# Optimization experiments

Hardware: AMD Instinct MI355X
Metric: run time of the kernel (lower is better)

The kernel has to match this reference:

```python
import jax, jax.numpy as jnp
import numpy as np

B, S, E, H, T, K, F = 2, 2048, 768, 12, 128, 16, 3072
DH = E // H


def _ln(x, s, b, eps=1e-6):
    mu = jnp.mean(x, axis=-1, keepdims=True)
    var = jnp.mean(jnp.square(x - mu), axis=-1, keepdims=True)
    return (x - mu) * jax.lax.rsqrt(var + eps) * s + b


def _forward(h, mask, W_topo, b_topo, W_m1, b_m1, W_m2, b_m2, ln_t_s, ln_t_b,
             W_p1, b_p1, W_p2, b_p2, ln1_s, ln1_b, Wq, Wk, Wv, W_gate, b_gate,
             W_o, b_o, ln2_s, ln2_b, W_f1, b_f1, W_f2, b_f2):
    # ---- TopologicalFeatureExtractor (on pre-LN hidden_states) ----
    topo = h @ W_topo + b_topo                                   # [B,S,T]
    hn = h / (jnp.linalg.norm(h, axis=-1, keepdims=True) + 1e-8)
    dist = 1.0 - jnp.einsum('bsd,btd->bst', hn, hn)              # cosine distance [B,S,S]
    dist = jnp.where(jnp.eye(S, dtype=bool)[None], 1e9, dist)    # mask self
    idx = jnp.argsort(dist, axis=-1)[:, :, :K]                   # k-NN indices [B,S,K]
    nd = jnp.take_along_axis(dist, idx, axis=-1)                 # [B,S,K]
    nf = jax.vmap(lambda t, i: t[i])(topo, idx)                  # gather neighbors [B,S,K,T]
    wts = jax.nn.softmax(-nd, axis=-1)[..., None]
    combined = topo + (nf * wts).sum(axis=2)
    t = jax.nn.relu(combined @ W_m1 + b_m1) @ W_m2 + b_m2
    t = _ln(t, ln_t_s, ln_t_b)
    pf = jax.nn.relu(t @ W_p1 + b_p1) @ W_p2 + b_p2              # persistence features [B,S,T]
    # ---- TopologicalAttention (pre-LN residual block) ----
    x = _ln(h, ln1_s, ln1_b)
    q = (x @ Wq).reshape(B, S, H, DH)
    k = (x @ Wk).reshape(B, S, H, DH)
    v = (x @ Wv).reshape(B, S, H, DH)
    scores = jnp.einsum('bqhd,bkhd->bhqk', q, k) / jnp.sqrt(jnp.asarray(DH, jnp.float32))
    scores = jnp.where(mask[:, None, None, :] == 0, -10000.0, scores)
    probs = jax.nn.softmax(scores, axis=-1)
    ctx = jnp.einsum('bhqk,bkhd->bqhd', probs, v).reshape(B, S, E)
    gate = jax.nn.sigmoid(jnp.concatenate([ctx, pf], axis=-1) @ W_gate + b_gate)
    ctx = gate * ctx + (1.0 - gate) * x                          # x is attention's input (post-LN)
    h = h + (ctx @ W_o + b_o)
    # ---- FFN block ----
    y = _ln(h, ln2_s, ln2_b)
    y = jax.nn.gelu(y @ W_f1 + b_f1, approximate=True)
    return h + (y @ W_f2 + b_f2)


def setup_inputs() -> dict:
    key = jax.random.key(0)
    ks = jax.random.split(key, 16)
    w = lambda k, shp: (0.02 * jax.random.normal(k, shp)).astype(jnp.float32)
    z = lambda shp: jnp.zeros(shp, jnp.float32)
    o = lambda shp: jnp.ones(shp, jnp.float32)
    return {
        'hidden_states': jax.random.normal(ks[0], (B, S, E), jnp.float32),
        'attention_mask': jnp.ones((B, S), jnp.int32),
        'W_topo': w(ks[1], (E, T)), 'b_topo': z((T,)),
        'W_m1': w(ks[2], (T, 2 * T)), 'b_m1': z((2 * T,)),
        'W_m2': w(ks[3], (2 * T, T)), 'b_m2': z((T,)),
        'ln_t_s': o((T,)), 'ln_t_b': z((T,)),
        'W_p1': w(ks[4], (T, T)), 'b_p1': z((T,)),
        'W_p2': w(ks[5], (T, T)), 'b_p2': z((T,)),
        'ln1_s': o((E,)), 'ln1_b': z((E,)),
        'Wq': w(ks[6], (E, E)), 'Wk': w(ks[7], (E, E)), 'Wv': w(ks[8], (E, E)),
        'W_gate': w(ks[9], (E + T, E)), 'b_gate': z((E,)),
        'W_o': w(ks[10], (E, E)), 'b_o': z((E,)),
        'ln2_s': o((E,)), 'ln2_b': z((E,)),
        'W_f1': w(ks[11], (E, F)), 'b_f1': z((F,)),
        'W_f2': w(ks[12], (F, E)), 'b_f2': z((E,)),
    }


def reference(hidden_states, attention_mask, W_topo, b_topo, W_m1, b_m1, W_m2, b_m2,
              ln_t_s, ln_t_b, W_p1, b_p1, W_p2, b_p2, ln1_s, ln1_b, Wq, Wk, Wv,
              W_gate, b_gate, W_o, b_o, ln2_s, ln2_b, W_f1, b_f1, W_f2, b_f2):
    return _forward(hidden_states, attention_mask, W_topo, b_topo, W_m1, b_m1, W_m2, b_m2,
                    ln_t_s, ln_t_b, W_p1, b_p1, W_p2, b_p2, ln1_s, ln1_b, Wq, Wk, Wv,
                    W_gate, b_gate, W_o, b_o, ln2_s, ln2_b, W_f1, b_f1, W_f2, b_f2)
```

## Files before the change

kernel.cpp:

```cpp
#include <hip/hip_runtime.h>
#include <hip/hip_bf16.h>
#include <math.h>

#define BDIM 2
#define SDIM 2048
#define EDIM 768
#define HDIM 12
#define TDIM 128
#define KNN  16
#define FDIM 3072
#define DHD  64
#define BS   (BDIM*SDIM)

typedef __attribute__((ext_vector_type(8))) short short8;
typedef __attribute__((ext_vector_type(4))) float f32x4;

__device__ __forceinline__ short f2bf(float f) {
  unsigned u = __float_as_uint(f);
  u = u + 0x7fff + ((u >> 16) & 1);
  return (short)(u >> 16);
}
__device__ __forceinline__ float bf2f(short s) {
  return __uint_as_float(((unsigned)(unsigned short)s) << 16);
}
__device__ __forceinline__ void cp16(void* lds, const void* g) {
  __builtin_amdgcn_global_load_lds(
      (const __attribute__((address_space(1))) unsigned int*)g,
      (__attribute__((address_space(3))) unsigned int*)lds, 16, 0, 0);
}

__device__ __forceinline__ void block_reduce_sum2(float& a, float& b) {
  __shared__ float sa[4], sb[4];
  #pragma unroll
  for (int off = 32; off > 0; off >>= 1) {
    a += __shfl_xor(a, off);
    b += __shfl_xor(b, off);
  }
  int wid = threadIdx.x >> 6;
  if ((threadIdx.x & 63) == 0) { sa[wid] = a; sb[wid] = b; }
  __syncthreads();
  a = sa[0] + sa[1] + sa[2] + sa[3];
  b = sb[0] + sb[1] + sb[2] + sb[3];
}

__global__ __launch_bounds__(256) void cvt_bf_kernel(
    const float* __restrict__ in, short* __restrict__ outp, int n8) {
  int i = blockIdx.x*256 + threadIdx.x;
  if (i < n8) {
    const float4* p4 = (const float4*)(in + (size_t)i*8);
    float4 a = p4[0], b = p4[1];
    short8 pk;
    pk[0]=f2bf(a.x); pk[1]=f2bf(a.y); pk[2]=f2bf(a.z); pk[3]=f2bf(a.w);
    pk[4]=f2bf(b.x); pk[5]=f2bf(b.y); pk[6]=f2bf(b.z); pk[7]=f2bf(b.w);
    *(short8*)(outp + (size_t)i*8) = pk;
  }
}

__global__ __launch_bounds__(256) void wconv_kernel(
    const float* __restrict__ W, short* __restrict__ Wt, int K, int N) {
  __shared__ float tile[64][65];
  const int n0 = blockIdx.x*64, k0 = blockIdx.y*64;
  const int tid = threadIdx.x;
  for (int i = tid; i < 4096; i += 256) {
    int r = i>>6, c = i&63;
    tile[r][c] = W[(size_t)(k0+r)*N + n0 + c];
  }
  __syncthreads();
  for (int i = tid; i < 4096; i += 256) {
    int r = i>>6, c = i&63;
    Wt[(size_t)(n0+r)*K + k0 + c] = f2bf(tile[c][r]);
  }
}

__global__ __launch_bounds__(256) void vtrans_kernel(
    const short* __restrict__ qkv, short* __restrict__ vt) {
  __shared__ short t[64][72];
  const int s0 = blockIdx.x*64;
  const int bh = blockIdx.y;
  const int b = bh / HDIM, h = bh % HDIM;
  const int tid = threadIdx.x;
  for (int i = tid; i < 512; i += 256) {
    int r = i>>3, c8 = (i&7)<<3;
    *(short8*)&t[r][c8] =
        *(const short8*)&qkv[(size_t)(b*SDIM+s0+r)*2304 + 1536 + h*DHD + c8];
  }
  __syncthreads();
  for (int i = tid; i < 512; i += 256) {
    int d = i>>3, c8 = (i&7)<<3;
    short8 pk;
    #pragma unroll
    for (int j = 0; j < 8; ++j) pk[j] = t[c8+j][d];
    *(short8*)&vt[(size_t)(bh*DHD+d)*SDIM + s0 + c8] = pk;
  }
}

__global__ __launch_bounds__(256) void norm_ln1_kernel(
    const float* __restrict__ h, const float* __restrict__ s,
    const float* __restrict__ bb, short* __restrict__ hh, short* __restrict__ hl,
    float* __restrict__ x, short* __restrict__ xb) {
  int row = blockIdx.x;
  const float* hr = h + (size_t)row * EDIM;
  float v[3], s1 = 0.f, s2 = 0.f;
  #pragma unroll
  for (int t = 0; t < 3; ++t) {
    v[t] = hr[threadIdx.x + 256*t];
    s1 += v[t]; s2 += v[t]*v[t];
  }
  block_reduce_sum2(s1, s2);
  float mu  = s1 * (1.f/EDIM);
  float var = s2 * (1.f/EDIM) - mu*mu;
  float rs  = rsqrtf(var + 1e-6f);
  float invn = 1.f / (sqrtf(s2) + 1e-8f);
  #pragma unroll
  for (int t = 0; t < 3; ++t) {
    int i = threadIdx.x + 256*t;
    size_t idx = (size_t)row*EDIM + i;
    float hnv = v[t]*invn;
    short hi = f2bf(hnv);
    hh[idx] = hi;
    hl[idx] = f2bf(hnv - bf2f(hi));
    float xv = (v[t]-mu)*rs*s[i] + bb[i];
    x[idx] = xv;
    xb[idx] = f2bf(xv);
  }
}

__global__ __launch_bounds__(256) void ln_bf_kernel(
    const float* __restrict__ in, const float* __restrict__ s,
    const float* __restrict__ bb, short* __restrict__ outb) {
  int row = blockIdx.x;
  const float* r = in + (size_t)row * EDIM;
  float v[3], s1 = 0.f, s2 = 0.f;
  #pragma unroll
  for (int t = 0; t < 3; ++t) {
    v[t] = r[threadIdx.x + 256*t];
    s1 += v[t]; s2 += v[t]*v[t];
  }
  block_reduce_sum2(s1, s2);
  float mu  = s1 * (1.f/EDIM);
  float var = s2 * (1.f/EDIM) - mu*mu;
  float rs  = rsqrtf(var + 1e-6f);
  #pragma unroll
  for (int t = 0; t < 3; ++t) {
    int i = threadIdx.x + 256*t;
    outb[(size_t)row*EDIM + i] = f2bf((v[t]-mu)*rs*s[i] + bb[i]);
  }
}

template<int ACT, int OUTBF>
__global__ __launch_bounds__(256) void gemm_mfma(
    const short* __restrict__ A, const short* __restrict__ Wt,
    const float* __restrict__ bias, const float* res,
    float* Cf, short* Cb, int Cb_ld,
    const float* __restrict__ blc, const float* __restrict__ blx,
    int K, int N) {
  __shared__ __align__(16) short As[128*64];
  __shared__ __align__(16) short Bs[128*64];
  const int bm = blockIdx.y*128, bn = blockIdx.x*128;
  const int tid = threadIdx.x;
  const int w = tid>>6, lane = tid&63, l15 = lane&15, g = lane>>4;
  const int wm = (w>>1)*64, wn = (w&1)*64;
  f32x4 acc[4][4] = {};
  for (int k0 = 0; k0 < K; k0 += 64) {
    #pragma unroll
    for (int it = 0; it < 4; ++it) {
      int p = (it*256 + tid)*16;
      int row = p >> 7;
      int slot = (p >> 4) & 7;
      int ss = slot ^ (row & 7);
      cp16((char*)As + it*4096 + w*1024, A  + (size_t)(bm+row)*K + k0 + ss*8);
      cp16((char*)Bs + it*4096 + w*1024, Wt + (size_t)(bn+row)*K + k0 + ss*8);
    }
    __syncthreads();
    #pragma unroll
    for (int ks = 0; ks < 2; ++ks) {
      short8 af[4], bfv[4];
      #pragma unroll
      for (int mt = 0; mt < 4; ++mt) {
        int r = wm + mt*16 + l15;
        af[mt] = *(const short8*)&As[r*64 + (((ks*4+g) ^ (r&7))*8)];
      }
      #pragma unroll
      for (int nt = 0; nt < 4; ++nt) {
        int r = wn + nt*16 + l15;
        bfv[nt] = *(const short8*)&Bs[r*64 + (((ks*4+g) ^ (r&7))*8)];
      }
      #pragma unroll
      for (int mt = 0; mt < 4; ++mt)
        #pragma unroll
        for (int nt = 0; nt < 4; ++nt)
          acc[mt][nt] = __builtin_amdgcn_mfma_f32_16x16x32_bf16(af[mt], bfv[nt], acc[mt][nt], 0, 0, 0);
    }
    __syncthreads();
  }
  #pragma unroll
  for (int mt = 0; mt < 4; ++mt) {
    #pragma unroll
    for (int nt = 0; nt < 4; ++nt) {
      #pragma unroll
      for (int reg = 0; reg < 4; ++reg) {
        int row = bm + wm + mt*16 + g*4 + reg;
        int col = bn + wn + nt*16 + l15;
        float v = acc[mt][nt][reg];
        if (bias) v += bias[col];
        if (ACT == 2) {
          float xx = v;
          float t2 = 0.7978845608028654f*(xx + 0.044715f*xx*xx*xx);
          v = 0.5f*xx*(1.f + tanhf(t2));
        }
        if (ACT == 3) {
          float gg = 1.f/(1.f + expf(-v));
          size_t ix = (size_t)row*EDIM + col;
          float mv = gg*blc[ix] + (1.f-gg)*blx[ix];
          Cb[(size_t)row*Cb_ld + col] = f2bf(mv);
        } else {
          if (res) v += res[(size_t)row*N + col];
          if (OUTBF) Cb[(size_t)row*Cb_ld + col] = f2bf(v);
          else       Cf[(size_t)row*N + col] = v;
        }
      }
    }
  }
}

__global__ __launch_bounds__(256) void dist_mfma(
    const short* __restrict__ Hh, const short* __restrict__ Hl,
    float* __restrict__ dist) {
  __shared__ __align__(16) short Ah[128*64], Al[128*64];
  __shared__ __align__(16) short Bh[128*64], Bl[128*64];
  const int bm = blockIdx.y*128, bn = blockIdx.x*128;
  const int tid = threadIdx.x;
  const int w = tid>>6, lane = tid&63, l15 = lane&15, g = lane>>4;
  const int wm = (w>>1)*64, wn = (w&1)*64;
  f32x4 acc[4][4] = {};
  for (int k0 = 0; k0 < EDIM; k0 += 64) {
    #pragma unroll
    for (int it = 0; it < 4; ++it) {
      int p = (it*256 + tid)*16;
      int row = p >> 7;
      int slot = (p >> 4) & 7;
      int ss = slot ^ (row & 7);
      size_t ga = (size_t)(bm+row)*EDIM + k0 + ss*8;
      size_t gb = (size_t)(bn+row)*EDIM + k0 + ss*8;
      cp16((char*)Ah + it*4096 + w*1024, Hh + ga);
      cp16((char*)Al + it*4096 + w*1024, Hl + ga);
      cp16((char*)Bh + it*4096 + w*1024, Hh + gb);
      cp16((char*)Bl + it*4096 + w*1024, Hl + gb);
    }
    __syncthreads();
    #pragma unroll
    for (int ks = 0; ks < 2; ++ks) {
      short8 ah[4], al[4], bh[4], bl[4];
      #pragma unroll
      for (int mt = 0; mt < 4; ++mt) {
        int r = wm + mt*16 + l15;
        int o = r*64 + (((ks*4+g) ^ (r&7))*8);
        ah[mt] = *(const short8*)&Ah[o];
        al[mt] = *(const short8*)&Al[o];
      }
      #pragma unroll
      for (int nt = 0; nt < 4; ++nt) {
        int r = wn + nt*16 + l15;
        int o = r*64 + (((ks*4+g) ^ (r&7))*8);
        bh[nt] = *(const short8*)&Bh[o];
        bl[nt] = *(const short8*)&Bl[o];
      }
      #pragma unroll
      for (int mt = 0; mt < 4; ++mt)
        #pragma unroll
        for (int nt = 0; nt < 4; ++nt) {
          acc[mt][nt] = __builtin_amdgcn_mfma_f32_16x16x32_bf16(ah[mt], bh[nt], acc[mt][nt], 0, 0, 0);
          acc[mt][nt] = __builtin_amdgcn_mfma_f32_16x16x32_bf16(ah[mt], bl[nt], acc[mt][nt], 0, 0, 0);
          acc[mt][nt] = __builtin_amdgcn_mfma_f32_16x16x32_bf16(al[mt], bh[nt], acc[mt][nt], 0, 0, 0);
        }
    }
    __syncthreads();
  }
  #pragma unroll
  for (int mt = 0; mt < 4; ++mt) {
    #pragma unroll
    for (int nt = 0; nt < 4; ++nt) {
      #pragma unroll
      for (int reg = 0; reg < 4; ++reg) {
        int row = bm + wm + mt*16 + g*4 + reg;
        int col = bn + wn + nt*16 + l15;
        float v = 1.f - acc[mt][nt][reg];
        if (row == col) v = 1e9f;
        dist[(size_t)row*SDIM + col] = v;
      }
    }
  }
}

__global__ __launch_bounds__(256) void topk_kernel(
    const float* __restrict__ dist, const float* __restrict__ topob,
    float* __restrict__ combb) {
  int s = blockIdx.x;
  __shared__ float wbv[4];
  __shared__ int   wbi[4];
  __shared__ float nd[KNN];
  __shared__ int   nidx[KNN];
  __shared__ float wts[KNN];
  const int tid = threadIdx.x, lane = tid & 63, wid = tid >> 6;
  const float* drow = dist + (size_t)s*SDIM;
  float lv[8];
  float best = 3e38f; int bidx = 1<<30;
  #pragma unroll
  for (int j = 0; j < 8; ++j) {
    int i = tid + j*256;
    float v = drow[i];
    lv[j] = v;
    if (v < best) { best = v; bidx = i; }
  }
  for (int pass = 0; pass < KNN; ++pass) {
    float bv = best; int bi = bidx;
    #pragma unroll
    for (int off = 32; off > 0; off >>= 1) {
      float ov = __shfl_xor(bv, off);
      int   oi = __shfl_xor(bi, off);
      if (ov < bv || (ov == bv && oi < bi)) { bv = ov; bi = oi; }
    }
    if (lane == 0) { wbv[wid] = bv; wbi[wid] = bi; }
    __syncthreads();
    if (tid == 0) {
      float fv = wbv[0]; int fi = wbi[0];
      #pragma unroll
      for (int q2 = 1; q2 < 4; ++q2)
        if (wbv[q2] < fv || (wbv[q2] == fv && wbi[q2] < fi)) { fv = wbv[q2]; fi = wbi[q2]; }
      nd[pass] = fv; nidx[pass] = fi;
    }
    __syncthreads();
    int wi = nidx[pass];
    if ((wi & 255) == tid) {
      int jj = wi >> 8;
      #pragma unroll
      for (int j = 0; j < 8; ++j) if (j == jj) lv[j] = 3e38f;
      best = 3e38f; bidx = 1<<30;
      #pragma unroll
      for (int j = 0; j < 8; ++j)
        if (lv[j] < best) { best = lv[j]; bidx = tid + j*256; }
    }
    __syncthreads();
  }
  if (tid == 0) {
    float m = -nd[0];
    for (int k2 = 1; k2 < KNN; ++k2) m = fmaxf(m, -nd[k2]);
    float ssum = 0.f;
    for (int k2 = 0; k2 < KNN; ++k2) { float e = expf(-nd[k2] - m); wts[k2] = e; ssum += e; }
    float inv = 1.f/ssum;
    for (int k2 = 0; k2 < KNN; ++k2) wts[k2] *= inv;
  }
  __syncthreads();
  if (tid < TDIM) {
    float acc = topob[(size_t)s*TDIM + tid];
    #pragma unroll
    for (int k2 = 0; k2 < KNN; ++k2) acc += wts[k2]*topob[(size_t)nidx[k2]*TDIM + tid];
    combb[(size_t)s*TDIM + tid] = acc;
  }
}

__global__ __launch_bounds__(256) void topo_mlp_kernel(
    const float* __restrict__ comb,
    const float* __restrict__ W1, const float* __restrict__ b1,
    const float* __restrict__ W2, const float* __restrict__ b2,
    const float* __restrict__ lns, const float* __restrict__ lnb,
    const float* __restrict__ Wp1, const float* __restrict__ bp1,
    const float* __restrict__ Wp2, const float* __restrict__ bp2,
    short* __restrict__ cat) {
  int row = blockIdx.x;
  __shared__ float c[TDIM], a1[2*TDIM], t2[TDIM];
  __shared__ float red[8];
  const int tid = threadIdx.x;
  if (tid < TDIM) c[tid] = comb[(size_t)row*TDIM + tid];
  __syncthreads();
  {
    float a = b1[tid];
    for (int i = 0; i < TDIM; ++i) a += c[i]*W1[i*2*TDIM + tid];
    a1[tid] = fmaxf(a, 0.f);
  }
  __syncthreads();
  float tval = 0.f;
  if (tid < TDIM) {
    float a = b2[tid];
    for (int i = 0; i < 2*TDIM; ++i) a += a1[i]*W2[i*TDIM + tid];
    tval = a;
  }
  float s1 = (tid < TDIM) ? tval : 0.f;
  float s2 = (tid < TDIM) ? tval*tval : 0.f;
  #pragma unroll
  for (int off = 32; off > 0; off >>= 1) { s1 += __shfl_xor(s1, off); s2 += __shfl_xor(s2, off); }
  if ((tid & 63) == 0) { red[tid>>6] = s1; red[4 + (tid>>6)] = s2; }
  __syncthreads();
  s1 = red[0]+red[1]+red[2]+red[3];
  s2 = red[4]+red[5]+red[6]+red[7];
  float mu  = s1 * (1.f/TDIM);
  float var = s2 * (1.f/TDIM) - mu*mu;
  float rs  = rsqrtf(var + 1e-6f);
  if (tid < TDIM) t2[tid] = (tval - mu)*rs*lns[tid] + lnb[tid];
  __syncthreads();
  if (tid < TDIM) {
    float a = bp1[tid];
    for (int i = 0; i < TDIM; ++i) a += t2[i]*Wp1[i*TDIM + tid];
    a1[tid] = fmaxf(a, 0.f);
  }
  __syncthreads();
  if (tid < TDIM) {
    float a = bp2[tid];
    for (int i = 0; i < TDIM; ++i) a += a1[i]*Wp2[i*TDIM + tid];
    cat[(size_t)row*896 + 768 + tid] = f2bf(a);
  }
}

__global__ __launch_bounds__(256) void attn_mfma(
    const short* __restrict__ qkv, const short* __restrict__ vtb,
    const int* __restrict__ maskp,
    float* __restrict__ ctx, short* __restrict__ ctxb) {
  __shared__ __align__(16) short Ks[128*64];
  __shared__ __align__(16) short Vs[64*128];
  __shared__ __align__(16) short Ps[4*16*128];
  __shared__ float Ms[128];
  const int qb0 = blockIdx.x*64;
  const int hh = blockIdx.y, b = blockIdx.z;
  const int bh = b*HDIM + hh;
  const int tid = threadIdx.x;
  const int w = tid>>6, lane = tid&63, l15 = lane&15, g = lane>>4;
  short8 qf[2];
  {
    size_t rbase = (size_t)(b*SDIM + qb0 + w*16 + l15)*2304 + hh*DHD;
    qf[0] = *(const short8*)&qkv[rbase + g*8];
    qf[1] = *(const short8*)&qkv[rbase + 32 + g*8];
  }
  f32x4 acc[4] = {};
  float m4[4] = {-1e30f, -1e30f, -1e30f, -1e30f};
  float l4[4] = {};
  for (int kt = 0; kt < SDIM; kt += 128) {
    #pragma unroll
    for (int it = 0; it < 4; ++it) {
      int t = it*256 + tid;
      int row = t>>3, slot = t&7, ss = slot ^ (row&7);
      cp16((char*)Ks + it*4096 + w*1024,
           qkv + (size_t)(b*SDIM+kt+row)*2304 + 768 + hh*DHD + ss*8);
    }
    #pragma unroll
    for (int it = 0; it < 4; ++it) {
      int t = it*256 + tid;
      int row = t>>4, slot = t&15, ss = slot ^ (row&15);
      cp16((char*)Vs + it*4096 + w*1024,
           vtb + (size_t)(bh*DHD+row)*SDIM + kt + ss*8);
    }
    if (tid < 128) Ms[tid] = (float)maskp[b*SDIM + kt + tid];
    __syncthreads();
    f32x4 s[8] = {};
    #pragma unroll
    for (int ks = 0; ks < 2; ++ks) {
      #pragma unroll
      for (int ct = 0; ct < 8; ++ct) {
        int r = ct*16 + l15;
        short8 kb8 = *(const short8*)&Ks[r*64 + (((ks*4+g) ^ (r&7))*8)];
        s[ct] = __builtin_amdgcn_mfma_f32_16x16x32_bf16(qf[ks], kb8, s[ct], 0, 0, 0);
      }
    }
    #pragma unroll
    for (int ct = 0; ct < 8; ++ct) {
      float mk = Ms[ct*16 + l15];
      #pragma unroll
      for (int reg = 0; reg < 4; ++reg) {
        float val = s[ct][reg]*0.125f;
        if (mk == 0.f) val = -10000.f;
        s[ct][reg] = val;
      }
    }
    #pragma unroll
    for (int reg = 0; reg < 4; ++reg) {
      float rm = -1e30f;
      #pragma unroll
      for (int ct = 0; ct < 8; ++ct) rm = fmaxf(rm, s[ct][reg]);
      #pragma unroll
      for (int off = 1; off < 16; off <<= 1) rm = fmaxf(rm, __shfl_xor(rm, off));
      float mnew = fmaxf(m4[reg], rm);
      float corr = __expf(m4[reg] - mnew);
      int qr = g*4 + reg;
      float rs = 0.f;
      #pragma unroll
      for (int ct = 0; ct < 8; ++ct) {
        float p = __expf(s[ct][reg] - mnew);
        rs += p;
        int col = ct*16 + l15;
        Ps[w*2048 + qr*128 + (((col>>3) ^ qr)<<3) + (col&7)] = f2bf(p);
      }
      #pragma unroll
      for (int off = 1; off < 16; off <<= 1) rs += __shfl_xor(rs, off);
      l4[reg] = l4[reg]*corr + rs;
      m4[reg] = mnew;
      #pragma unroll
      for (int dt = 0; dt < 4; ++dt) acc[dt][reg] *= corr;
    }
    #pragma unroll
    for (int ks2 = 0; ks2 < 4; ++ks2) {
      short8 pa = *(const short8*)&Ps[w*2048 + l15*128 + (((ks2*4+g) ^ l15)*8)];
      #pragma unroll
      for (int dt = 0; dt < 4; ++dt) {
        int r = dt*16 + l15;
        short8 vb8 = *(const short8*)&Vs[r*128 + (((ks2*4+g) ^ (r&15))*8)];
        acc[dt] = __builtin_amdgcn_mfma_f32_16x16x32_bf16(pa, vb8, acc[dt], 0, 0, 0);
      }
    }
    __syncthreads();
  }
  float inv[4];
  #pragma unroll
  for (int reg = 0; reg < 4; ++reg) inv[reg] = 1.f / l4[reg];
  #pragma unroll
  for (int dt = 0; dt < 4; ++dt) {
    #pragma unroll
    for (int reg = 0; reg < 4; ++reg) {
      int row = b*SDIM + qb0 + w*16 + g*4 + reg;
      float v = acc[dt][reg]*inv[reg];
      ctx [(size_t)row*EDIM + hh*DHD + dt*16 + l15] = v;
      ctxb[(size_t)row*896  + hh*DHD + dt*16 + l15] = f2bf(v);
    }
  }
}

extern "C" void kernel_launch(void* const* d_in, const int* in_sizes, int n_in,
                              void* d_out, int out_size, void* d_ws, size_t ws_size,
                              hipStream_t stream) {
  const float* h      = (const float*)d_in[0];
  const int*   mask   = (const int*)  d_in[1];
  const float* W_topo = (const float*)d_in[2];
  const float* b_topo = (const float*)d_in[3];
  const float* W_m1   = (const float*)d_in[4];
  const float* b_m1   = (const float*)d_in[5];
  const float* W_m2   = (const float*)d_in[6];
  const float* b_m2   = (const float*)d_in[7];
  const float* ln_t_s = (const float*)d_in[8];
  const float* ln_t_b = (const float*)d_in[9];
  const float* W_p1   = (const float*)d_in[10];
  const float* b_p1   = (const float*)d_in[11];
  const float* W_p2   = (const float*)d_in[12];
  const float* b_p2   = (const float*)d_in[13];
  const float* ln1_s  = (const float*)d_in[14];
  const float* ln1_b  = (const float*)d_in[15];
  const float* Wq     = (const float*)d_in[16];
  const float* Wk     = (const float*)d_in[17];
  const float* Wv     = (const float*)d_in[18];
  const float* W_gate = (const float*)d_in[19];
  const float* b_gate = (const float*)d_in[20];
  const float* W_o    = (const float*)d_in[21];
  const float* b_o    = (const float*)d_in[22];
  const float* ln2_s  = (const float*)d_in[23];
  const float* ln2_b  = (const float*)d_in[24];
  const float* W_f1   = (const float*)d_in[25];
  const float* b_f1   = (const float*)d_in[26];
  const float* W_f2   = (const float*)d_in[27];
  const float* b_f2   = (const float*)d_in[28];
  float* out = (float*)d_out;

  const size_t R = (size_t)BS*EDIM;
  short* wt_topo = (short*)d_ws;
  short* wt_qkv  = wt_topo + (size_t)128*768;
  short* wt_g    = wt_qkv  + (size_t)2304*768;
  short* wt_o    = wt_g    + (size_t)768*896;
  short* wt_f1   = wt_o    + (size_t)768*768;
  short* wt_f2   = wt_f1   + (size_t)3072*768;
  short* regA    = wt_f2   + (size_t)768*3072;
  short* regBCE  = regA + R;
  short* regD    = regBCE + 3*R;
  short* cat     = regD + R;
  float* xf      = (float*)(cat + (size_t)BS*896);
  float* Ff      = xf + R;
  short* vtb     = (short*)(Ff + (size_t)SDIM*SDIM);

  short* h_bf  = regA;
  short* mixb  = regA;
  short* hn_hi = regBCE;
  short* hn_lo = regBCE + R;
  float* topo  = (float*)(regBCE + 2*R);
  float* comb  = topo + (size_t)BS*TDIM;
  short* qkvb  = regBCE;
  short* x_bf  = regD;
  short* y_bf  = regD;
  float* dbuf  = Ff;
  float* ctxf  = Ff;
  short* ybuf  = (short*)Ff;

  cvt_bf_kernel<<<(BS*EDIM/8 + 255)/256, 256, 0, stream>>>(h, h_bf, BS*EDIM/8);
  wconv_kernel<<<dim3(TDIM/64, EDIM/64), 256, 0, stream>>>(W_topo, wt_topo, EDIM, TDIM);
  wconv_kernel<<<dim3(EDIM/64, EDIM/64), 256, 0, stream>>>(Wq, wt_qkv, EDIM, EDIM);
  wconv_kernel<<<dim3(EDIM/64, EDIM/64), 256, 0, stream>>>(Wk, wt_qkv + (size_t)768*768, EDIM, EDIM);
  wconv_kernel<<<dim3(EDIM/64, EDIM/64), 256, 0, stream>>>(Wv, wt_qkv + (size_t)1536*768, EDIM, EDIM);
  wconv_kernel<<<dim3(EDIM/64, 896/64), 256, 0, stream>>>(W_gate, wt_g, 896, EDIM);
  wconv_kernel<<<dim3(EDIM/64, EDIM/64), 256, 0, stream>>>(W_o, wt_o, EDIM, EDIM);
  wconv_kernel<<<dim3(FDIM/64, EDIM/64), 256, 0, stream>>>(W_f1, wt_f1, EDIM, FDIM);
  wconv_kernel<<<dim3(EDIM/64, FDIM/64), 256, 0, stream>>>(W_f2, wt_f2, FDIM, EDIM);
  norm_ln1_kernel<<<BS, 256, 0, stream>>>(h, ln1_s, ln1_b, hn_hi, hn_lo, xf, x_bf);
  gemm_mfma<0,0><<<dim3(1, BS/128), 256, 0, stream>>>(
      h_bf, wt_topo, b_topo, nullptr, topo, nullptr, 0, nullptr, nullptr, EDIM, TDIM);
  for (int b = 0; b < BDIM; ++b) {
    dist_mfma<<<dim3(SDIM/128, SDIM/128), 256, 0, stream>>>(
        hn_hi + (size_t)b*SDIM*EDIM, hn_lo + (size_t)b*SDIM*EDIM, dbuf);
    topk_kernel<<<SDIM, 256, 0, stream>>>(
        dbuf, topo + (size_t)b*SDIM*TDIM, comb + (size_t)b*SDIM*TDIM);
  }
  topo_mlp_kernel<<<BS, 256, 0, stream>>>(comb, W_m1, b_m1, W_m2, b_m2,
                                          ln_t_s, ln_t_b, W_p1, b_p1, W_p2, b_p2, cat);
  gemm_mfma<0,1><<<dim3(2304/128, BS/128), 256, 0, stream>>>(
      x_bf, wt_qkv, nullptr, nullptr, nullptr, qkvb, 2304, nullptr, nullptr, EDIM, 2304);
  vtrans_kernel<<<dim3(SDIM/64, BDIM*HDIM), 256, 0, stream>>>(qkvb, vtb);
  attn_mfma<<<dim3(SDIM/64, HDIM, BDIM), 256, 0, stream>>>(qkvb, vtb, mask, ctxf, cat);
  gemm_mfma<3,1><<<dim3(EDIM/128, BS/128), 256, 0, stream>>>(
      cat, wt_g, b_gate, nullptr, nullptr, mixb, EDIM, ctxf, xf, 896, EDIM);
  gemm_mfma<0,0><<<dim3(EDIM/128, BS/128), 256, 0, stream>>>(
      mixb, wt_o, b_o, h, out, nullptr, 0, nullptr, nullptr, EDIM, EDIM);
  ln_bf_kernel<<<BS, 256, 0, stream>>>(out, ln2_s, ln2_b, y_bf);
  gemm_mfma<2,1><<<dim3(FDIM/128, BS/128), 256, 0, stream>>>(
      y_bf, wt_f1, b_f1, nullptr, nullptr, ybuf, FDIM, nullptr, nullptr, EDIM, FDIM);
  gemm_mfma<0,0><<<dim3(EDIM/128, BS/128), 256, 0, stream>>>(
      ybuf, wt_f2, b_f2, out, out, nullptr, 0, nullptr, nullptr, FDIM, EDIM);
}
```

Before: 749.2 us.

## Batch weight conversions, fold bf16 cast into LN1, streamline attention softmax

Merges the eight weight transpose-convert launches into one segmented kernel, and folds the fp32-to-bf16 cast of the hidden states into the norm/LN1 kernel. Rewrites the attention softmax to work in the exp2 domain with a pre-scaled log2e factor, using packed bf16 conversion and transposed MFMA operands. Each lane now owns a single query row, and the running-max rescale is skipped when the new max is within a threshold. The aim is to cut launch overhead, one extra pass over the input, and softmax ALU and shuffle cost. The lazy rescale threshold adds some numerical risk.

After: 688.5 us. -8.1%, faster.

```diff
diff --git a/kernel.cpp b/kernel.cpp
--- a/kernel.cpp
+++ b/kernel.cpp
@@ -14,6 +14,7 @@
 
 typedef __attribute__((ext_vector_type(8))) short short8;
 typedef __attribute__((ext_vector_type(4))) float f32x4;
+typedef __attribute__((ext_vector_type(2))) unsigned u32x2;
 
 __device__ __forceinline__ short f2bf(float f) {
   unsigned u = __float_as_uint(f);
@@ -23,6 +24,16 @@
 __device__ __forceinline__ float bf2f(short s) {
   return __uint_as_float(((unsigned)(unsigned short)s) << 16);
 }
+__device__ __forceinline__ unsigned cvt_pk_bf16(float a, float b) {
+  unsigned r;
+  asm("v_cvt_pk_bf16_f32 %0, %1, %2" : "=v"(r) : "v"(a), "v"(b));
+  return r;
+}
+__device__ __forceinline__ float exp2_fast(float x) {
+  float r;
+  asm("v_exp_f32 %0, %1" : "=v"(r) : "v"(x));
+  return r;
+}
 __device__ __forceinline__ void cp16(void* lds, const void* g) {
   __builtin_amdgcn_global_load_lds(
       (const __attribute__((address_space(1))) unsigned int*)g,
@@ -43,23 +54,20 @@
   b = sb[0] + sb[1] + sb[2] + sb[3];
 }
 
-__global__ __launch_bounds__(256) void cvt_bf_kernel(
-    const float* __restrict__ in, short* __restrict__ outp, int n8) {
-  int i = blockIdx.x*256 + threadIdx.x;
-  if (i < n8) {
-    const float4* p4 = (const float4*)(in + (size_t)i*8);
-    float4 a = p4[0], b = p4[1];
-    short8 pk;
-    pk[0]=f2bf(a.x); pk[1]=f2bf(a.y); pk[2]=f2bf(a.z); pk[3]=f2bf(a.w);
-    pk[4]=f2bf(b.x); pk[5]=f2bf(b.y); pk[6]=f2bf(b.z); pk[7]=f2bf(b.w);
-    *(short8*)(outp + (size_t)i*8) = pk;
-  }
-}
-
-__global__ __launch_bounds__(256) void wconv_kernel(
-    const float* __restrict__ W, short* __restrict__ Wt, int K, int N) {
+struct WcSeg { const float* src; short* dst; int K, N, ntx, start; };
+struct WcArgs { WcSeg s[8]; };
+
+__global__ __launch_bounds__(256) void wconv_all(WcArgs a) {
   __shared__ float tile[64][65];
-  const int n0 = blockIdx.x*64, k0 = blockIdx.y*64;
+  const int bid = blockIdx.x;
+  int si = 0;
+  #pragma unroll
+  for (int i = 1; i < 8; ++i) if (bid >= a.s[i].start) si = i;
+  const float* W = a.s[si].src;
+  short* Wt = a.s[si].dst;
+  const int K = a.s[si].K, N = a.s[si].N;
+  const int t = bid - a.s[si].start;
+  const int n0 = (t % a.s[si].ntx)*64, k0 = (t / a.s[si].ntx)*64;
   const int tid = threadIdx.x;
   for (int i = tid; i < 4096; i += 256) {
     int r = i>>6, c = i&63;
@@ -96,7 +104,8 @@
 
 __global__ __launch_bounds__(256) void norm_ln1_kernel(
     const float* __restrict__ h, const float* __restrict__ s,
-    const float* __restrict__ bb, short* __restrict__ hh, short* __restrict__ hl,
+    const float* __restrict__ bb, short* __restrict__ hb,
+    short* __restrict__ hh, short* __restrict__ hl,
     float* __restrict__ x, short* __restrict__ xb) {
   int row = blockIdx.x;
   const float* hr = h + (size_t)row * EDIM;
@@ -115,6 +124,7 @@
   for (int t = 0; t < 3; ++t) {
     int i = threadIdx.x + 256*t;
     size_t idx = (size_t)row*EDIM + i;
+    hb[idx] = f2bf(v[t]);
     float hnv = v[t]*invn;
     short hi = f2bf(hnv);
     hh[idx] = hi;
@@ -419,6 +429,8 @@
   __shared__ __align__(16) short Vs[64*128];
   __shared__ __align__(16) short Ps[4*16*128];
   __shared__ float Ms[128];
+  const float SCL = 0.18033688011112042f;
+  const float MASKVAL = -14426.950408889634f;
   const int qb0 = blockIdx.x*64;
   const int hh = blockIdx.y, b = blockIdx.z;
   const int bh = b*HDIM + hh;
@@ -431,8 +443,9 @@
     qf[1] = *(const short8*)&qkv[rbase + 32 + g*8];
   }
   f32x4 acc[4] = {};
-  float m4[4] = {-1e30f, -1e30f, -1e30f, -1e30f};
-  float l4[4] = {};
+  float m_run = -1e30f, l_run = 0.f;
+  char* PsW = (char*)Ps + w*4096 + l15*256;
+  const int swz = (l15 & 7) << 1;
   for (int kt = 0; kt < SDIM; kt += 128) {
     #pragma unroll
     for (int it = 0; it < 4; ++it) {
@@ -457,47 +470,55 @@
       for (int ct = 0; ct < 8; ++ct) {
         int r = ct*16 + l15;
         short8 kb8 = *(const short8*)&Ks[r*64 + (((ks*4+g) ^ (r&7))*8)];
-        s[ct] = __builtin_amdgcn_mfma_f32_16x16x32_bf16(qf[ks], kb8, s[ct], 0, 0, 0);
-      }
-    }
+        s[ct] = __builtin_amdgcn_mfma_f32_16x16x32_bf16(kb8, qf[ks], s[ct], 0, 0, 0);
+      }
+    }
+    float rm = -1e30f;
     #pragma unroll
     for (int ct = 0; ct < 8; ++ct) {
-      float mk = Ms[ct*16 + l15];
+      float4 mk = *(const float4*)&Ms[ct*16 + g*4];
+      float v0 = s[ct][0]*SCL; if (mk.x == 0.f) v0 = MASKVAL;
+      float v1 = s[ct][1]*SCL; if (mk.y == 0.f) v1 = MASKVAL;
+      float v2 = s[ct][2]*SCL; if (mk.z == 0.f) v2 = MASKVAL;
+      float v3 = s[ct][3]*SCL; if (mk.w == 0.f) v3 = MASKVAL;
+      s[ct][0] = v0; s[ct][1] = v1; s[ct][2] = v2; s[ct][3] = v3;
+      rm = fmaxf(rm, fmaxf(fmaxf(v0, v1), fmaxf(v2, v3)));
+    }
+    rm = fmaxf(rm, __shfl_xor(rm, 16));
+    rm = fmaxf(rm, __shfl_xor(rm, 32));
+    if (__any(rm > m_run + 11.5415603f)) {
+      float mnew = fmaxf(m_run, rm);
+      float corr = exp2_fast(m_run - mnew);
+      l_run *= corr;
       #pragma unroll
       for (int reg = 0; reg < 4; ++reg) {
-        float val = s[ct][reg]*0.125f;
-        if (mk == 0.f) val = -10000.f;
-        s[ct][reg] = val;
-      }
-    }
-    #pragma unroll
-    for (int reg = 0; reg < 4; ++reg) {
-      float rm = -1e30f;
-      #pragma unroll
-      for (int ct = 0; ct < 8; ++ct) rm = fmaxf(rm, s[ct][reg]);
-      #pragma unroll
-      for (int off = 1; off < 16; off <<= 1) rm = fmaxf(rm, __shfl_xor(rm, off));
-      float mnew = fmaxf(m4[reg], rm);
-      float corr = __expf(m4[reg] - mnew);
-      int qr = g*4 + reg;
-      float rs = 0.f;
-      #pragma unroll
-      for (int ct = 0; ct < 8; ++ct) {
-        float p = __expf(s[ct][reg] - mnew);
-        rs += p;
-        int col = ct*16 + l15;
-        Ps[w*2048 + qr*128 + (((col>>3) ^ qr)<<3) + (col&7)] = f2bf(p);
-      }
-      #pragma unroll
-      for (int off = 1; off < 16; off <<= 1) rs += __shfl_xor(rs, off);
-      l4[reg] = l4[reg]*corr + rs;
-      m4[reg] = mnew;
-      #pragma unroll
-      for (int dt = 0; dt < 4; ++dt) acc[dt][reg] *= corr;
-    }
+        float cq = __shfl(corr, (g<<4) | (g*4 + reg));
+        #pragma unroll
+        for (int dt = 0; dt < 4; ++dt) acc[dt][reg] *= cq;
+      }
+      m_run = mnew;
+    }
+    float rs = 0.f;
+    #pragma unroll
+    for (int ct = 0; ct < 8; ++ct) {
+      float p0 = exp2_fast(s[ct][0] - m_run);
+      float p1 = exp2_fast(s[ct][1] - m_run);
+      float p2 = exp2_fast(s[ct][2] - m_run);
+      float p3 = exp2_fast(s[ct][3] - m_run);
+      rs += (p0 + p1) + (p2 + p3);
+      u32x2 pk;
+      pk.x = cvt_pk_bf16(p0, p1);
+      pk.y = cvt_pk_bf16(p2, p3);
+      int slot = ct*4 + g;
+      *(u32x2*)(PsW + ((slot ^ swz) << 3)) = pk;
+    }
+    rs += __shfl_xor(rs, 16);
+    rs += __shfl_xor(rs, 32);
+    l_run += rs;
     #pragma unroll
     for (int ks2 = 0; ks2 < 4; ++ks2) {
-      short8 pa = *(const short8*)&Ps[w*2048 + l15*128 + (((ks2*4+g) ^ l15)*8)];
+      int s0 = ks2*8 + g*2;
+      short8 pa = *(const short8*)(PsW + ((s0 ^ swz) << 3));
       #pragma unroll
       for (int dt = 0; dt < 4; ++dt) {
         int r = dt*16 + l15;
@@ -507,15 +528,16 @@
     }
     __syncthreads();
   }
-  float inv[4];
-  #pragma unroll
-  for (int reg = 0; reg < 4; ++reg) inv[reg] = 1.f / l4[reg];
+  float invq[4];
+  #pragma unroll
+  for (int reg = 0; reg < 4; ++reg)
+    invq[reg] = 1.f / __shfl(l_run, (g<<4) | (g*4 + reg));
   #pragma unroll
   for (int dt = 0; dt < 4; ++dt) {
     #pragma unroll
     for (int reg = 0; reg < 4; ++reg) {
       int row = b*SDIM + qb0 + w*16 + g*4 + reg;
-      float v = acc[dt][reg]*inv[reg];
+      float v = acc[dt][reg]*invq[reg];
       ctx [(size_t)row*EDIM + hh*DHD + dt*16 + l15] = v;
       ctxb[(size_t)row*896  + hh*DHD + dt*16 + l15] = f2bf(v);
     }
@@ -584,16 +606,17 @@
   float* ctxf  = Ff;
   short* ybuf  = (short*)Ff;
 
-  cvt_bf_kernel<<<(BS*EDIM/8 + 255)/256, 256, 0, stream>>>(h, h_bf, BS*EDIM/8);
-  wconv_kernel<<<dim3(TDIM/64, EDIM/64), 256, 0, stream>>>(W_topo, wt_topo, EDIM, TDIM);
-  wconv_kernel<<<dim3(EDIM/64, EDIM/64), 256, 0, stream>>>(Wq, wt_qkv, EDIM, EDIM);
-  wconv_kernel<<<dim3(EDIM/64, EDIM/64), 256, 0, stream>>>(Wk, wt_qkv + (size_t)768*768, EDIM, EDIM);
-  wconv_kernel<<<dim3(EDIM/64, EDIM/64), 256, 0, stream>>>(Wv, wt_qkv + (size_t)1536*768, EDIM, EDIM);
-  wconv_kernel<<<dim3(EDIM/64, 896/64), 256, 0, stream>>>(W_gate, wt_g, 896, EDIM);
-  wconv_kernel<<<dim3(EDIM/64, EDIM/64), 256, 0, stream>>>(W_o, wt_o, EDIM, EDIM);
-  wconv_kernel<<<dim3(FDIM/64, EDIM/64), 256, 0, stream>>>(W_f1, wt_f1, EDIM, FDIM);
-  wconv_kernel<<<dim3(EDIM/64, FDIM/64), 256, 0, stream>>>(W_f2, wt_f2, FDIM, EDIM);
-  norm_ln1_kernel<<<BS, 256, 0, stream>>>(h, ln1_s, ln1_b, hn_hi, hn_lo, xf, x_bf);
+  WcArgs wa;
+  wa.s[0] = {W_topo, wt_topo,                    EDIM, TDIM,  TDIM/64, 0};
+  wa.s[1] = {Wq,     wt_qkv,                     EDIM, EDIM,  EDIM/64, 24};
+  wa.s[2] = {Wk,     wt_qkv + (size_t)768*768,   EDIM, EDIM,  EDIM/64, 168};
+  wa.s[3] = {Wv,     wt_qkv + (size_t)1536*768,  EDIM, EDIM,  EDIM/64, 312};
+  wa.s[4] = {W_gate, wt_g,                       896,  EDIM,  EDIM/64, 456};
+  wa.s[5] = {W_o,    wt_o,                       EDIM, EDIM,  EDIM/64, 624};
+  wa.s[6] = {W_f1,   wt_f1,                      EDIM, FDIM,  FDIM/64, 768};
+  wa.s[7] = {W_f2,   wt_f2,                      FDIM, EDIM,  EDIM/64, 1344};
+  wconv_all<<<1920, 256, 0, stream>>>(wa);
+  norm_ln1_kernel<<<BS, 256, 0, stream>>>(h, ln1_s, ln1_b, h_bf, hn_hi, hn_lo, xf, x_bf);
   gemm_mfma<0,0><<<dim3(1, BS/128), 256, 0, stream>>>(
       h_bf, wt_topo, b_topo, nullptr, topo, nullptr, 0, nullptr, nullptr, EDIM, TDIM);
   for (int b = 0; b < BDIM; ++b) {
```
